# Performance work log

Hardware: AMD Instinct MI355X
Metric: run time of the kernel (lower is better)

Reference implementation:

```python
import math
import jax, jax.numpy as jnp
import numpy as np

N, B, C, H, K = 1024, 8, 512, 8, 5  # seq len, batch, d_model, heads, near_kth
NEG = -1.0e9


def setup_inputs() -> dict:
    key = jax.random.key(0)
    ks = jax.random.split(key, 10)
    s = 0.02
    return {
        "query": jax.random.normal(ks[0], (N, B, C), jnp.float32),
        "key_t": jax.random.normal(ks[1], (N, B, C), jnp.float32),
        "value": jax.random.normal(ks[2], (N, B, C), jnp.float32),
        "src_position": jax.random.normal(ks[3], (N, B, 3), jnp.float32),
        "tgt_position": jax.random.normal(ks[4], (N, B, 3), jnp.float32),
        # nn.MultiheadAttention params (in_proj split into q/k/v, plus out_proj)
        "Wq": jax.random.normal(ks[5], (C, C), jnp.float32) * s,
        "Wk": jax.random.normal(ks[6], (C, C), jnp.float32) * s,
        "Wv": jax.random.normal(ks[7], (C, C), jnp.float32) * s,
        "bq": jnp.zeros((C,), jnp.float32),
        "bk": jnp.zeros((C,), jnp.float32),
        "bv": jnp.zeros((C,), jnp.float32),
        "Wo": jax.random.normal(ks[8], (C, C), jnp.float32) * s,
        "bo": jnp.zeros((C,), jnp.float32),
    }


def reference(query, key_t, value, src_position, tgt_position,
              Wq, Wk, Wv, bq, bk, bv, Wo, bo):
    # --- 'nearby' positional mask ---------------------------------------
    # dist[b, tgt, src] = ||src_position[src,b] - tgt_position[tgt,b]||^2
    diff = src_position[None, :, :, :] - tgt_position[:, None, :, :]  # (Nt,Ns,B,3)
    dist = jnp.sum(diff * diff, axis=-1).transpose(2, 0, 1)           # (B,Nt,Ns)
    # torch: topk(dist, k=5, dim=1, largest=False) -> 5 nearest TARGETS per source
    _, idx = jax.lax.top_k(-dist.transpose(0, 2, 1), K)               # (B,Ns,K) tgt idx
    mask = jnp.full((B, N, N), NEG, jnp.float32)
    b_i = jnp.arange(B)[:, None, None]
    s_i = jnp.arange(N)[None, :, None]
    mask = mask.at[b_i, idx, s_i].set(0.0)                            # (B,Nt,Ns)

    # --- multihead attention (eval mode, dropout=0) ----------------------
    hd = C // H
    scale = 1.0 / math.sqrt(hd)
    q = ((query @ Wq.T + bq) * scale).reshape(N, B, H, hd)
    k = (key_t @ Wk.T + bk).reshape(N, B, H, hd)
    v = (value @ Wv.T + bv).reshape(N, B, H, hd)
    scores = jnp.einsum('tbhd,sbhd->bhts', q, k) + mask[:, None]      # (B,H,Nt,Ns)
    attn = jax.nn.softmax(scores, axis=-1)
    ctx = jnp.einsum('bhts,sbhd->tbhd', attn, v).reshape(N, B, C)
    out = ctx @ Wo.T + bo                                             # (N,B,C)
    attn_avg = attn.mean(axis=1)                                      # (B,Nt,Ns)
    return out, attn_avg
```

## Files before the change

kernel.cpp:

```cpp
#include <hip/hip_runtime.h>
#include <cstdint>
#include <cstddef>

#define NSEQ 1024
#define BATCH 8
#define CMODEL 512
#define NHEAD 8
#define HDIM 64
#define CAP 64
#define FLTMAX 3.402823466e+38f

typedef short bf16x8 __attribute__((ext_vector_type(8)));
typedef float f32x4 __attribute__((ext_vector_type(4)));
typedef unsigned short ushort8v __attribute__((ext_vector_type(8)));
typedef unsigned short ushort2v __attribute__((ext_vector_type(2)));

__device__ inline unsigned short f2bf(float f) {
    unsigned int u = __builtin_bit_cast(unsigned int, f);
    u += 0x7fffu + ((u >> 16) & 1u);
    return (unsigned short)(u >> 16);
}
__device__ inline float bf2f(unsigned short u) {
    return __builtin_bit_cast(float, (unsigned int)u << 16);
}

#define GLDS16(gsrc, ldst) \
    __builtin_amdgcn_global_load_lds((const __attribute__((address_space(1))) void*)(gsrc), \
                                     (__attribute__((address_space(3))) void*)(ldst), 16, 0, 0)

__global__ __launch_bounds__(256) void prepA(const float* __restrict__ w0,
                                             const float* __restrict__ w1,
                                             const float* __restrict__ w2,
                                             const float* __restrict__ w3,
                                             const float* __restrict__ value,
                                             const float* __restrict__ tgtp,
                                             const float* __restrict__ srcp,
                                             unsigned short* __restrict__ o0,
                                             unsigned short* __restrict__ o1,
                                             unsigned short* __restrict__ o2,
                                             unsigned short* __restrict__ o3,
                                             unsigned int* __restrict__ zp,
                                             float* __restrict__ vm_raw,
                                             float* __restrict__ tgt_soa,
                                             float* __restrict__ src_soa) {
    const int bid = blockIdx.x;
    const int tid = threadIdx.x;
    if (bid < 512) {
        const int idx = bid * 256 + tid;
        const int seg = idx >> 15;
        const int c   = idx & 32767;
        const float* src = seg == 0 ? w0 : seg == 1 ? w1 : seg == 2 ? w2 : w3;
        unsigned short* dst = seg == 0 ? o0 : seg == 1 ? o1 : seg == 2 ? o2 : o3;
        const float4 v0 = *(const float4*)(src + (size_t)c * 8);
        const float4 v1 = *(const float4*)(src + (size_t)c * 8 + 4);
        ushort8v u;
        u[0] = f2bf(v0.x); u[1] = f2bf(v0.y); u[2] = f2bf(v0.z); u[3] = f2bf(v0.w);
        u[4] = f2bf(v1.x); u[5] = f2bf(v1.y); u[6] = f2bf(v1.z); u[7] = f2bf(v1.w);
        *(ushort8v*)(dst + (size_t)c * 8) = u;
        return;
    }
    if (bid < 544) {
        zp[(bid - 512) * 256 + tid] = 0u;
        return;
    }
    if (bid < 608) {
        const int cb = bid - 544;
        const int b = cb >> 3, cg = cb & 7;
        const int ts = tid >> 6, c = cg * 64 + (tid & 63);
        float s = 0.f;
        for (int i = 0; i < 256; ++i) {
            const int t = ts * 256 + i;
            s += value[((size_t)t * BATCH + b) * CMODEL + c];
        }
        __shared__ float sh[4][64];
        sh[ts][tid & 63] = s;
        __syncthreads();
        if (ts == 0)
            vm_raw[b * CMODEL + c] = sh[0][tid & 63] + sh[1][tid & 63] +
                                     sh[2][tid & 63] + sh[3][tid & 63];
        return;
    }
    const int tb = bid - 608;
    const int which = tb >> 3, b = tb & 7;
    const float* src = which == 0 ? tgtp : srcp;
    float* dst = which == 0 ? tgt_soa : src_soa;
    for (int t = tid; t < NSEQ; t += 256) {
        const float* p = src + ((size_t)t * BATCH + b) * 3;
        dst[(b * 3 + 0) * NSEQ + t] = p[0];
        dst[(b * 3 + 1) * NSEQ + t] = p[1];
        dst[(b * 3 + 2) * NSEQ + t] = p[2];
    }
}

__global__ __launch_bounds__(256) void megaB(const float* __restrict__ a0,
                                             const float* __restrict__ a1,
                                             const float* __restrict__ a2,
                                             unsigned short* __restrict__ oa0,
                                             unsigned short* __restrict__ oa1,
                                             unsigned short* __restrict__ oa2,
                                             const float* __restrict__ src_soa,
                                             const float* __restrict__ tgt_soa,
                                             int* __restrict__ row_cnt,
                                             int* __restrict__ row_list,
                                             const unsigned short* __restrict__ Wv,
                                             const float* __restrict__ bv,
                                             const float* __restrict__ vm_raw,
                                             float* __restrict__ vm) {
    const int p = blockIdx.x;
    const int tid = threadIdx.x;

    if (p < 8) {
        const int bsel = p;
        const int c0 = tid * 2;
        float s0 = 0.f, s1 = 0.f;
        const unsigned short* w0r = Wv + (size_t)c0 * CMODEL;
        const unsigned short* w1r = w0r + CMODEL;
        const float* vr = vm_raw + bsel * CMODEL;
        for (int k8 = 0; k8 < 64; ++k8) {
            const ushort8v w0 = *(const ushort8v*)(w0r + k8 * 8);
            const ushort8v w1 = *(const ushort8v*)(w1r + k8 * 8);
            const float4 va = *(const float4*)(vr + k8 * 8);
            const float4 vb = *(const float4*)(vr + k8 * 8 + 4);
            s0 += va.x * bf2f(w0[0]) + va.y * bf2f(w0[1]) + va.z * bf2f(w0[2]) + va.w * bf2f(w0[3])
                + vb.x * bf2f(w0[4]) + vb.y * bf2f(w0[5]) + vb.z * bf2f(w0[6]) + vb.w * bf2f(w0[7]);
            s1 += va.x * bf2f(w1[0]) + va.y * bf2f(w1[1]) + va.z * bf2f(w1[2]) + va.w * bf2f(w1[3])
                + vb.x * bf2f(w1[4]) + vb.y * bf2f(w1[5]) + vb.z * bf2f(w1[6]) + vb.w * bf2f(w1[7]);
        }
        vm[bsel * CMODEL + c0]     = s0 * (1.f / (float)NSEQ) + bv[c0];
        vm[bsel * CMODEL + c0 + 1] = s1 * (1.f / (float)NSEQ) + bv[c0 + 1];
        return;
    }

    if (p >= 2056) {
        const unsigned int idx = (unsigned int)(p - 2056) * 256u + tid;
        const unsigned int seg = idx >> 19;
        const unsigned int c   = idx & 524287u;
        const float* src = seg == 0 ? a0 : seg == 1 ? a1 : a2;
        unsigned short* dst = seg == 0 ? oa0 : seg == 1 ? oa1 : oa2;
        const float4 v0 = *(const float4*)(src + (size_t)c * 8);
        const float4 v1 = *(const float4*)(src + (size_t)c * 8 + 4);
        ushort8v u;
        u[0] = f2bf(v0.x); u[1] = f2bf(v0.y); u[2] = f2bf(v0.z); u[3] = f2bf(v0.w);
        u[4] = f2bf(v1.x); u[5] = f2bf(v1.y); u[6] = f2bf(v1.z); u[7] = f2bf(v1.w);
        *(ushort8v*)(dst + (size_t)c * 8) = u;
        return;
    }

    const int w = tid >> 6, lane = tid & 63;
    const int wg = (p - 8) * 4 + w;
    const int s = wg & 1023, b = wg >> 10;

    const float* tx = tgt_soa + (b * 3 + 0) * NSEQ;
    const float* ty = tgt_soa + (b * 3 + 1) * NSEQ;
    const float* tz = tgt_soa + (b * 3 + 2) * NSEQ;
    const float sx = src_soa[(b * 3 + 0) * NSEQ + s];
    const float sy = src_soa[(b * 3 + 1) * NSEQ + s];
    const float sz = src_soa[(b * 3 + 2) * NSEQ + s];

    float dv[16];
    #pragma unroll
    for (int i = 0; i < 16; ++i) {
        const int t = i * 64 + lane;
        const float dx = tx[t] - sx;
        const float dy = ty[t] - sy;
        const float dz = tz[t] - sz;
        dv[i] = dx * dx + dy * dy + dz * dz;
    }

    #pragma unroll
    for (int k = 0; k < 5; ++k) {
        float bvv = FLTMAX;
        int   bii = 0x7fffffff;
        #pragma unroll
        for (int i = 0; i < 16; ++i) {
            if (dv[i] < bvv) { bvv = dv[i]; bii = i * 64 + lane; }
        }
        #pragma unroll
        for (int off = 1; off < 64; off <<= 1) {
            const float ov = __shfl_xor(bvv, off);
            const int   oi = __shfl_xor(bii, off);
            if (ov < bvv || (ov == bvv && oi < bii)) { bvv = ov; bii = oi; }
        }
        if (lane == (bii & 63)) {
            #pragma unroll
            for (int i = 0; i < 16; ++i)
                if (bii == i * 64 + lane) dv[i] = FLTMAX;
        }
        if (lane == 0) {
            const int pos = atomicAdd(&row_cnt[b * NSEQ + bii], 1);
            if (pos < CAP) row_list[((size_t)b * NSEQ + bii) * CAP + pos] = s;
        }
    }
}

__global__ __launch_bounds__(256, 3) void gemm_proj(const unsigned short* __restrict__ Aq,
                                                    const unsigned short* __restrict__ Ak,
                                                    const unsigned short* __restrict__ Av,
                                                    const unsigned short* __restrict__ Wq,
                                                    const unsigned short* __restrict__ Wk,
                                                    const unsigned short* __restrict__ Wv,
                                                    const float* __restrict__ bq,
                                                    const float* __restrict__ bk,
                                                    const float* __restrict__ bv,
                                                    unsigned short* __restrict__ oq,
                                                    unsigned short* __restrict__ ok,
                                                    unsigned short* __restrict__ ov) {
    __shared__ __align__(16) unsigned short smem[3 * 8192];
    const int p = blockIdx.x;
    const int logical = (p & 7) * 96 + (p >> 3);
    const int z = logical >> 8;
    const int r = logical & 255;
    const int m0 = (r >> 2) * 128, n0 = (r & 3) * 128;
    const unsigned short* Abf = z == 0 ? Aq : z == 1 ? Ak : Av;
    const unsigned short* Wbf = z == 0 ? Wq : z == 1 ? Wk : Wv;
    const float* bias = z == 0 ? bq : z == 1 ? bk : bv;
    unsigned short* outp = z == 0 ? oq : z == 1 ? ok : ov;
    const float scale = z == 0 ? 0.125f : 1.0f;

    const int tid = threadIdx.x;
    const int l = tid & 63, w = tid >> 6;
    const int wr = (w >> 1) * 64, wc = (w & 1) * 64;
    const int lr = l & 15, g = l >> 4;

    f32x4 acc[4][4] = {};

    const int rowX = tid >> 2;
    const int kg0  = (tid & 3) ^ ((rowX >> 1) & 3);
    const unsigned short* aS0 = Abf + (size_t)(m0 + rowX) * CMODEL + kg0 * 8;
    const unsigned short* aS1 = aS0 + (size_t)64 * CMODEL;
    const unsigned short* bS0 = Wbf + (size_t)(n0 + rowX) * CMODEL + kg0 * 8;
    const unsigned short* bS1 = bS0 + (size_t)64 * CMODEL;
    const int wb = w * 512;

    auto STAGE = [&](int k0, int buf) {
        unsigned short* bb = smem + buf * 8192;
        GLDS16(aS0 + k0, bb + wb);
        GLDS16(aS1 + k0, bb + 2048 + wb);
        GLDS16(bS0 + k0, bb + 4096 + wb);
        GLDS16(bS1 + k0, bb + 6144 + wb);
    };
    auto COMPUTE = [&](const unsigned short* base) {
        bf16x8 af[4], bg[4];
        #pragma unroll
        for (int i = 0; i < 4; ++i) {
            const int ra = wr + i * 16 + lr;
            af[i] = *(const bf16x8*)(base + ra * 32 + ((g ^ ((ra >> 1) & 3)) << 3));
        }
        #pragma unroll
        for (int j = 0; j < 4; ++j) {
            const int rb = wc + j * 16 + lr;
            bg[j] = *(const bf16x8*)(base + 4096 + rb * 32 + ((g ^ ((rb >> 1) & 3)) << 3));
        }
        #pragma unroll
        for (int i = 0; i < 4; ++i)
            #pragma unroll
            for (int j = 0; j < 4; ++j)
                acc[i][j] = __builtin_amdgcn_mfma_f32_16x16x32_bf16(af[i], bg[j], acc[i][j], 0, 0, 0);
    };

    STAGE(0, 0);
    STAGE(32, 1);

    int cur = 0;
    for (int t = 0; t < 15; ++t) {
        asm volatile("s_waitcnt vmcnt(4)" ::: "memory");
        __builtin_amdgcn_s_barrier();
        if (t < 14) {
            int nb = cur + 2; if (nb >= 3) nb -= 3;
            STAGE((t + 2) * 32, nb);
        }
        COMPUTE(smem + cur * 8192);
        ++cur; if (cur == 3) cur = 0;
    }
    asm volatile("s_waitcnt vmcnt(0)" ::: "memory");
    __builtin_amdgcn_s_barrier();
    COMPUTE(smem + cur * 8192);

    #pragma unroll
    for (int i = 0; i < 4; ++i) {
        #pragma unroll
        for (int j = 0; j < 4; ++j) {
            const int col = n0 + wc + j * 16 + lr;
            const float bcol = bias[col];
            #pragma unroll
            for (int rr = 0; rr < 4; ++rr) {
                const int row = m0 + wr + i * 16 + g * 4 + rr;
                const float val = (acc[i][j][rr] + bcol) * scale;
                const int t = row >> 3, bb = row & 7;
                outp[((size_t)(bb * NSEQ + t)) * CMODEL + col] = f2bf(val);
            }
        }
    }
}

__global__ __launch_bounds__(256, 3) void gemm_out(const unsigned short* __restrict__ Abf,
                                                   const unsigned short* __restrict__ Wbf,
                                                   const float* __restrict__ bias,
                                                   float* __restrict__ out) {
    __shared__ __align__(16) unsigned short smem[3 * 6144];
    const int p = blockIdx.x;
    const int logical = (p & 7) * 64 + (p >> 3);
    const int m0 = (logical >> 3) * 128, n0 = (logical & 7) * 64;

    const int tid = threadIdx.x;
    const int l = tid & 63, w = tid >> 6;
    const int wr = (w >> 1) * 64, wc = (w & 1) * 32;
    const int lr = l & 15, g = l >> 4;

    f32x4 acc[4][2] = {};

    const int rowX = tid >> 2;
    const int kg0  = (tid & 3) ^ ((rowX >> 1) & 3);
    const unsigned short* aS0 = Abf + (size_t)(m0 + rowX) * CMODEL + kg0 * 8;
    const unsigned short* aS1 = aS0 + (size_t)64 * CMODEL;
    const unsigned short* bS0 = Wbf + (size_t)(n0 + rowX) * CMODEL + kg0 * 8;
    const int wb = w * 512;

    auto STAGE = [&](int k0, int buf) {
        unsigned short* bb = smem + buf * 6144;
        GLDS16(aS0 + k0, bb + wb);
        GLDS16(aS1 + k0, bb + 2048 + wb);
        GLDS16(bS0 + k0, bb + 4096 + wb);
    };
    auto COMPUTE = [&](const unsigned short* base) {
        bf16x8 af[4], bg[2];
        #pragma unroll
        for (int i = 0; i < 4; ++i) {
            const int ra = wr + i * 16 + lr;
            af[i] = *(const bf16x8*)(base + ra * 32 + ((g ^ ((ra >> 1) & 3)) << 3));
        }
        #pragma unroll
        for (int j = 0; j < 2; ++j) {
            const int rb = wc + j * 16 + lr;
            bg[j] = *(const bf16x8*)(base + 4096 + rb * 32 + ((g ^ ((rb >> 1) & 3)) << 3));
        }
        #pragma unroll
        for (int i = 0; i < 4; ++i)
            #pragma unroll
            for (int j = 0; j < 2; ++j)
                acc[i][j] = __builtin_amdgcn_mfma_f32_16x16x32_bf16(af[i], bg[j], acc[i][j], 0, 0, 0);
    };

    STAGE(0, 0);
    STAGE(32, 1);

    int cur = 0;
    for (int t = 0; t < 15; ++t) {
        asm volatile("s_waitcnt vmcnt(3)" ::: "memory");
        __builtin_amdgcn_s_barrier();
        if (t < 14) {
            int nb = cur + 2; if (nb >= 3) nb -= 3;
            STAGE((t + 2) * 32, nb);
        }
        COMPUTE(smem + cur * 6144);
        ++cur; if (cur == 3) cur = 0;
    }
    asm volatile("s_waitcnt vmcnt(0)" ::: "memory");
    __builtin_amdgcn_s_barrier();
    COMPUTE(smem + cur * 6144);

    #pragma unroll
    for (int i = 0; i < 4; ++i) {
        #pragma unroll
        for (int j = 0; j < 2; ++j) {
            const int col = n0 + wc + j * 16 + lr;
            const float bcol = bias[col];
            #pragma unroll
            for (int r = 0; r < 4; ++r) {
                const int row = m0 + wr + i * 16 + g * 4 + r;
                out[(size_t)row * CMODEL + col] = acc[i][j][r] + bcol;
            }
        }
    }
}

__global__ __launch_bounds__(256) void sparse_attn(const unsigned short* __restrict__ q_ws,
                                                   const unsigned short* __restrict__ k_ws,
                                                   const unsigned short* __restrict__ v_ws,
                                                   const int* __restrict__ row_cnt,
                                                   const int* __restrict__ row_list,
                                                   const float* __restrict__ vm,
                                                   unsigned short* __restrict__ ctx,
                                                   float* __restrict__ attn_out) {
    const int t = blockIdx.x;
    const int b = blockIdx.y;
    const int tid = threadIdx.x;

    int cnt = row_cnt[b * NSEQ + t];
    if (cnt > CAP) cnt = CAP;

    float* arow = attn_out + ((size_t)b * NSEQ + t) * NSEQ;

    if (cnt == 0) {
        const float u = 1.f / (float)NSEQ;
        const float4 uv = {u, u, u, u};
        ((float4*)arow)[tid] = uv;
        for (int c = tid; c < CMODEL; c += 256)
            ctx[((size_t)t * BATCH + b) * CMODEL + c] = f2bf(vm[b * CMODEL + c]);
        return;
    }

    {
        const float4 zv = {0.f, 0.f, 0.f, 0.f};
        ((float4*)arow)[tid] = zv;
    }

    __shared__ float qs[CMODEL];
    __shared__ float esc[CAP][8];
    __shared__ float denom[8];
    __shared__ int   slist[CAP];

    if (tid < 8) denom[tid] = 0.f;
    if (tid < cnt) slist[tid] = row_list[((size_t)b * NSEQ + t) * CAP + tid];
    {
        const ushort2v qv = *(const ushort2v*)(q_ws + ((size_t)b * NSEQ + t) * CMODEL + tid * 2);
        qs[tid * 2] = bf2f(qv[0]); qs[tid * 2 + 1] = bf2f(qv[1]);
    }
    __syncthreads();

    const int wid = tid >> 6, lane = tid & 63;
    for (int i = wid; i < cnt; i += 4) {
        const int s = slist[i];
        const ushort8v kv = *(const ushort8v*)(k_ws + ((size_t)b * NSEQ + s) * CMODEL + lane * 8);
        const float* qrow = qs + lane * 8;
        float part = 0.f;
        #pragma unroll
        for (int j = 0; j < 8; ++j) part += qrow[j] * bf2f(kv[j]);
        part += __shfl_xor(part, 1);
        part += __shfl_xor(part, 2);
        part += __shfl_xor(part, 4);
        if ((lane & 7) == 0) {
            const int h = lane >> 3;
            const float e = __expf(part);
            esc[i][h] = e;
            atomicAdd(&denom[h], e);
        }
    }
    __syncthreads();

    for (int x = tid; x < cnt * 8; x += 256)
        esc[x >> 3][x & 7] /= denom[x & 7];
    __syncthreads();

    for (int i = tid; i < cnt; i += 256) {
        float pm = 0.f;
        #pragma unroll
        for (int h = 0; h < 8; ++h) pm += esc[i][h];
        arow[slist[i]] = pm * 0.125f;
    }

    const int c0 = tid * 2;
    const int h0 = c0 >> 6;
    float acc0 = 0.f, acc1 = 0.f;
    for (int i = 0; i < cnt; ++i) {
        const int s = slist[i];
        const float p = esc[i][h0];
        const ushort2v vv = *(const ushort2v*)(v_ws + ((size_t)b * NSEQ + s) * CMODEL + c0);
        acc0 += p * bf2f(vv[0]); acc1 += p * bf2f(vv[1]);
    }
    unsigned short* crow = ctx + ((size_t)t * BATCH + b) * CMODEL;
    ushort2v cv; cv[0] = f2bf(acc0); cv[1] = f2bf(acc1);
    *(ushort2v*)(crow + c0) = cv;
}

extern "C" void kernel_launch(void* const* d_in, const int* in_sizes, int n_in,
                              void* d_out, int out_size, void* d_ws, size_t ws_size,
                              hipStream_t stream) {
    (void)in_sizes; (void)n_in; (void)out_size; (void)ws_size;

    const float* query = (const float*)d_in[0];
    const float* key_t = (const float*)d_in[1];
    const float* value = (const float*)d_in[2];
    const float* srcp  = (const float*)d_in[3];
    const float* tgtp  = (const float*)d_in[4];
    const float* Wq    = (const float*)d_in[5];
    const float* Wk    = (const float*)d_in[6];
    const float* Wv    = (const float*)d_in[7];
    const float* bq    = (const float*)d_in[8];
    const float* bk    = (const float*)d_in[9];
    const float* bv    = (const float*)d_in[10];
    const float* Wo    = (const float*)d_in[11];
    const float* bo    = (const float*)d_in[12];

    float* out      = (float*)d_out;
    float* attn_out = out + (size_t)NSEQ * BATCH * CMODEL;

    const size_t NBC = (size_t)BATCH * NSEQ * CMODEL;
    const size_t WSZ = (size_t)CMODEL * CMODEL;
    unsigned short* q_ws  = (unsigned short*)d_ws;
    unsigned short* k_ws  = q_ws + NBC;
    unsigned short* v_ws  = k_ws + NBC;
    unsigned short* ctxbf = v_ws + NBC;
    unsigned short* qbf   = ctxbf + NBC;
    unsigned short* kbf   = qbf + NBC;
    unsigned short* vbf   = kbf + NBC;
    unsigned short* wqbf  = vbf + NBC;
    unsigned short* wkbf  = wqbf + WSZ;
    unsigned short* wvbf  = wkbf + WSZ;
    unsigned short* wobf  = wvbf + WSZ;
    int*   row_cnt  = (int*)(wobf + WSZ);
    float* vm       = (float*)(row_cnt + BATCH * NSEQ);
    float* vm_raw   = vm + BATCH * CMODEL;
    float* tgt_soa  = vm_raw + BATCH * CMODEL;
    float* src_soa  = tgt_soa + (size_t)BATCH * 3 * NSEQ;
    int*   row_list = (int*)(src_soa + (size_t)BATCH * 3 * NSEQ);

    prepA<<<624, 256, 0, stream>>>(Wq, Wk, Wv, Wo, value, tgtp, srcp,
                                   wqbf, wkbf, wvbf, wobf,
                                   (unsigned int*)row_cnt, vm_raw,
                                   tgt_soa, src_soa);

    megaB<<<8200, 256, 0, stream>>>(query, key_t, value, qbf, kbf, vbf,
                                    src_soa, tgt_soa, row_cnt, row_list,
                                    wvbf, bv, vm_raw, vm);

    gemm_proj<<<768, 256, 0, stream>>>(qbf, kbf, vbf,
                                       wqbf, wkbf, wvbf,
                                       bq, bk, bv,
                                       q_ws, k_ws, v_ws);

    sparse_attn<<<dim3(NSEQ, BATCH), 256, 0, stream>>>(q_ws, k_ws, v_ws, row_cnt,
                                                       row_list, vm, ctxbf, attn_out);

    gemm_out<<<512, 256, 0, stream>>>(ctxbf, wobf, bo, out);
}
```

Before: 103.7 us.

## Replace iterative wave top-5 with packed-key per-lane sorted lists and merge network

The nearest-5 selection now packs each distance and its target index into a 64-bit key. Every lane keeps a sorted top-5 list with compare-exchange insertion, and the lanes then merge their lists through a butterfly shuffle followed by a small sorting network. This replaces five rounds of full 16-element scans plus 6-step shuffle reductions. Separately, the v-mean matvec is spread over 32 blocks with wave-level reductions instead of 8 blocks of per-thread serial loops. The packed key ordering relies on non-negative float bit patterns, and the tie-break by lower index is kept.

```diff
diff --git a/kernel.cpp b/kernel.cpp
--- a/kernel.cpp
+++ b/kernel.cpp
@@ -14,6 +14,7 @@
 typedef float f32x4 __attribute__((ext_vector_type(4)));
 typedef unsigned short ushort8v __attribute__((ext_vector_type(8)));
 typedef unsigned short ushort2v __attribute__((ext_vector_type(2)));
+typedef unsigned long long u64;
 
 __device__ inline unsigned short f2bf(float f) {
     unsigned int u = __builtin_bit_cast(unsigned int, f);
@@ -92,6 +93,9 @@
     }
 }
 
+#define CX64(a, b) { const bool _c = (a) < (b); const u64 _mn = _c ? (a) : (b); \
+                     const u64 _mx = _c ? (b) : (a); (a) = _mn; (b) = _mx; }
+
 __global__ __launch_bounds__(256) void megaB(const float* __restrict__ a0,
                                              const float* __restrict__ a1,
                                              const float* __restrict__ a2,
@@ -109,30 +113,28 @@
     const int p = blockIdx.x;
     const int tid = threadIdx.x;
 
-    if (p < 8) {
-        const int bsel = p;
-        const int c0 = tid * 2;
-        float s0 = 0.f, s1 = 0.f;
-        const unsigned short* w0r = Wv + (size_t)c0 * CMODEL;
-        const unsigned short* w1r = w0r + CMODEL;
+    if (p < 32) {
+        const int bsel = p >> 2, quad = p & 3;
+        const int w = tid >> 6, lane = tid & 63;
         const float* vr = vm_raw + bsel * CMODEL;
-        for (int k8 = 0; k8 < 64; ++k8) {
-            const ushort8v w0 = *(const ushort8v*)(w0r + k8 * 8);
-            const ushort8v w1 = *(const ushort8v*)(w1r + k8 * 8);
-            const float4 va = *(const float4*)(vr + k8 * 8);
-            const float4 vb = *(const float4*)(vr + k8 * 8 + 4);
-            s0 += va.x * bf2f(w0[0]) + va.y * bf2f(w0[1]) + va.z * bf2f(w0[2]) + va.w * bf2f(w0[3])
-                + vb.x * bf2f(w0[4]) + vb.y * bf2f(w0[5]) + vb.z * bf2f(w0[6]) + vb.w * bf2f(w0[7]);
-            s1 += va.x * bf2f(w1[0]) + va.y * bf2f(w1[1]) + va.z * bf2f(w1[2]) + va.w * bf2f(w1[3])
-                + vb.x * bf2f(w1[4]) + vb.y * bf2f(w1[5]) + vb.z * bf2f(w1[6]) + vb.w * bf2f(w1[7]);
-        }
-        vm[bsel * CMODEL + c0]     = s0 * (1.f / (float)NSEQ) + bv[c0];
-        vm[bsel * CMODEL + c0 + 1] = s1 * (1.f / (float)NSEQ) + bv[c0 + 1];
+        const float4 va = *(const float4*)(vr + lane * 8);
+        const float4 vb = *(const float4*)(vr + lane * 8 + 4);
+        float vp[8] = {va.x, va.y, va.z, va.w, vb.x, vb.y, vb.z, vb.w};
+        for (int i = 0; i < 32; ++i) {
+            const int c = quad * 128 + w * 32 + i;
+            const ushort8v wv = *(const ushort8v*)(Wv + (size_t)c * CMODEL + lane * 8);
+            float s = 0.f;
+            #pragma unroll
+            for (int j = 0; j < 8; ++j) s += vp[j] * bf2f(wv[j]);
+            #pragma unroll
+            for (int off = 1; off < 64; off <<= 1) s += __shfl_xor(s, off);
+            if (lane == 0) vm[bsel * CMODEL + c] = s * (1.f / (float)NSEQ) + bv[c];
+        }
         return;
     }
 
-    if (p >= 2056) {
-        const unsigned int idx = (unsigned int)(p - 2056) * 256u + tid;
+    if (p >= 2080) {
+        const unsigned int idx = (unsigned int)(p - 2080) * 256u + tid;
         const unsigned int seg = idx >> 19;
         const unsigned int c   = idx & 524287u;
         const float* src = seg == 0 ? a0 : seg == 1 ? a1 : a2;
@@ -147,7 +149,7 @@
     }
 
     const int w = tid >> 6, lane = tid & 63;
-    const int wg = (p - 8) * 4 + w;
+    const int wg = (p - 32) * 4 + w;
     const int s = wg & 1023, b = wg >> 10;
 
     const float* tx = tgt_soa + (b * 3 + 0) * NSEQ;
@@ -157,38 +159,48 @@
     const float sy = src_soa[(b * 3 + 1) * NSEQ + s];
     const float sz = src_soa[(b * 3 + 2) * NSEQ + s];
 
-    float dv[16];
+    u64 v0 = ~0ull, v1 = ~0ull, v2 = ~0ull, v3 = ~0ull, v4 = ~0ull;
+
     #pragma unroll
     for (int i = 0; i < 16; ++i) {
         const int t = i * 64 + lane;
         const float dx = tx[t] - sx;
         const float dy = ty[t] - sy;
         const float dz = tz[t] - sz;
-        dv[i] = dx * dx + dy * dy + dz * dz;
+        const float d = dx * dx + dy * dy + dz * dz;
+        u64 x = ((u64)__builtin_bit_cast(unsigned int, d) << 32) | (unsigned int)t;
+        if (x < v4) {
+            CX64(v0, x);
+            CX64(v1, x);
+            CX64(v2, x);
+            CX64(v3, x);
+            CX64(v4, x);
+        }
     }
 
     #pragma unroll
-    for (int k = 0; k < 5; ++k) {
-        float bvv = FLTMAX;
-        int   bii = 0x7fffffff;
-        #pragma unroll
-        for (int i = 0; i < 16; ++i) {
-            if (dv[i] < bvv) { bvv = dv[i]; bii = i * 64 + lane; }
-        }
-        #pragma unroll
-        for (int off = 1; off < 64; off <<= 1) {
-            const float ov = __shfl_xor(bvv, off);
-            const int   oi = __shfl_xor(bii, off);
-            if (ov < bvv || (ov == bvv && oi < bii)) { bvv = ov; bii = oi; }
-        }
-        if (lane == (bii & 63)) {
-            #pragma unroll
-            for (int i = 0; i < 16; ++i)
-                if (bii == i * 64 + lane) dv[i] = FLTMAX;
-        }
-        if (lane == 0) {
-            const int pos = atomicAdd(&row_cnt[b * NSEQ + bii], 1);
-            if (pos < CAP) row_list[((size_t)b * NSEQ + bii) * CAP + pos] = s;
+    for (int off = 1; off < 64; off <<= 1) {
+        const u64 p0 = __shfl_xor(v4, off);
+        const u64 p1 = __shfl_xor(v3, off);
+        const u64 p2 = __shfl_xor(v2, off);
+        const u64 p3 = __shfl_xor(v1, off);
+        const u64 p4 = __shfl_xor(v0, off);
+        v0 = v0 < p0 ? v0 : p0;
+        v1 = v1 < p1 ? v1 : p1;
+        v2 = v2 < p2 ? v2 : p2;
+        v3 = v3 < p3 ? v3 : p3;
+        v4 = v4 < p4 ? v4 : p4;
+        CX64(v0, v1); CX64(v3, v4); CX64(v2, v4); CX64(v2, v3); CX64(v1, v4);
+        CX64(v0, v3); CX64(v0, v2); CX64(v1, v3); CX64(v1, v2);
+    }
+
+    if (lane == 0) {
+        const u64 win[5] = {v0, v1, v2, v3, v4};
+        #pragma unroll
+        for (int k = 0; k < 5; ++k) {
+            const int tt = (int)(unsigned int)win[k];
+            const int pos = atomicAdd(&row_cnt[b * NSEQ + tt], 1);
+            if (pos < CAP) row_list[((size_t)b * NSEQ + tt) * CAP + pos] = s;
         }
     }
 }
@@ -510,7 +522,7 @@
                                    (unsigned int*)row_cnt, vm_raw,
                                    tgt_soa, src_soa);
 
-    megaB<<<8200, 256, 0, stream>>>(query, key_t, value, qbf, kbf, vbf,
+    megaB<<<8224, 256, 0, stream>>>(query, key_t, value, qbf, kbf, vbf,
                                     src_soa, tgt_soa, row_cnt, row_list,
                                     wvbf, bv, vm_raw, vm);
 
```

Result: faster. 94.37 us (-9.0%).
